# Performance work log

Measured on AMD Instinct MI355X. Metric: run time of the kernel, lower is better.

The kernel has to match this reference:

```python
import jax, jax.numpy as jnp
import numpy as np
import math

N_EMBD = 1024
N_HEAD = 16
HEAD_DIM = N_EMBD // N_HEAD
SEQ = 2048
BATCH = 2
EPS = 1e-5


def _gelu_tanh(x):
    c = math.sqrt(2.0 / math.pi)
    return 0.5 * x * (1.0 + jnp.tanh(c * (x + 0.044715 * x ** 3)))


def _layernorm(x, w, b):
    mean = jnp.mean(x, axis=-1, keepdims=True)
    var = jnp.mean(jnp.square(x - mean), axis=-1, keepdims=True)  # unbiased=False
    return (x - mean) / jnp.sqrt(var + EPS) * w + b


def setup_inputs() -> dict:
    key = jax.random.key(0)
    ks = jax.random.split(key, 8)
    D = N_EMBD
    s = 0.02
    return {
        "x": jax.random.normal(ks[0], (BATCH, SEQ, D), jnp.float32),
        "ln1_w": jnp.ones((D,), jnp.float32),
        "ln1_b": jnp.zeros((D,), jnp.float32),
        "w_qkv": jax.random.normal(ks[1], (D, 3 * D), jnp.float32) * s,
        "b_qkv": jnp.zeros((3 * D,), jnp.float32),
        "w_attn_proj": jax.random.normal(ks[2], (D, D), jnp.float32) * s,
        "b_attn_proj": jnp.zeros((D,), jnp.float32),
        "ln2_w": jnp.ones((D,), jnp.float32),
        "ln2_b": jnp.zeros((D,), jnp.float32),
        "w_fc": jax.random.normal(ks[3], (D, 4 * D), jnp.float32) * s,
        "b_fc": jnp.zeros((4 * D,), jnp.float32),
        "w_proj": jax.random.normal(ks[4], (4 * D, D), jnp.float32) * s,
        "b_proj": jnp.zeros((D,), jnp.float32),
    }


def reference(x, ln1_w, ln1_b, w_qkv, b_qkv, w_attn_proj, b_attn_proj,
              ln2_w, ln2_b, w_fc, b_fc, w_proj, b_proj):
    bs, T, D = x.shape
    # --- attention branch (pre-LN) ---
    h = _layernorm(x, ln1_w, ln1_b)
    qkv = h @ w_qkv + b_qkv                      # [B,T,3D]
    q, k, v = jnp.split(qkv, 3, axis=-1)
    q = q.reshape(bs, T, N_HEAD, HEAD_DIM).transpose(0, 2, 1, 3)  # [B,H,T,d]
    k = k.reshape(bs, T, N_HEAD, HEAD_DIM).transpose(0, 2, 1, 3)
    v = v.reshape(bs, T, N_HEAD, HEAD_DIM).transpose(0, 2, 1, 3)
    scores = jnp.einsum("bhqd,bhkd->bhqk", q, k) * (1.0 / math.sqrt(HEAD_DIM))
    causal = jnp.tril(jnp.ones((T, T), bool))
    scores = jnp.where(causal[None, None], scores, -jnp.inf)
    att = jax.nn.softmax(scores, axis=-1)
    ctx = jnp.einsum("bhqk,bhkd->bhqd", att, v)
    ctx = ctx.transpose(0, 2, 1, 3).reshape(bs, T, D)
    attn_out = ctx @ w_attn_proj + b_attn_proj
    x = x + attn_out
    # --- MLP branch (pre-LN) ---
    h = _layernorm(x, ln2_w, ln2_b)
    h = _gelu_tanh(h @ w_fc + b_fc)
    h = h @ w_proj + b_proj
    return x + h
```

## Files before the change

kernel.cpp:

```cpp
#include <hip/hip_runtime.h>

typedef unsigned short u16;
typedef __attribute__((ext_vector_type(8))) __bf16 bf16x8;
typedef __attribute__((ext_vector_type(8))) unsigned short ushort8;
typedef __attribute__((ext_vector_type(4))) float f32x4;

#define MFMA16(a, b, c) __builtin_amdgcn_mfma_f32_16x16x32_bf16((a), (b), (c), 0, 0, 0)

__device__ __forceinline__ u16 f2bf(float f) {
  union { __bf16 h; u16 u; } cv;
  cv.h = (__bf16)f;
  return cv.u;
}

__device__ __forceinline__ void async16(const u16* g, u16* l) {
  __builtin_amdgcn_global_load_lds(
      (const __attribute__((address_space(1))) void*)g,
      (__attribute__((address_space(3))) void*)l, 16, 0, 0);
}

__global__ __launch_bounds__(256)
void transpose_bf16(const float* __restrict__ W, u16* __restrict__ Wt, int K, int N) {
  __shared__ float t[32][33];
  const int n0 = blockIdx.x * 32, k0 = blockIdx.y * 32;
  const int tx = threadIdx.x, ty = threadIdx.y;
  #pragma unroll
  for (int i = 0; i < 32; i += 8)
    t[ty + i][tx] = W[(size_t)(k0 + ty + i) * N + n0 + tx];
  __syncthreads();
  #pragma unroll
  for (int i = 0; i < 32; i += 8)
    Wt[(size_t)(n0 + ty + i) * K + k0 + tx] = f2bf(t[tx][ty + i]);
}

__global__ __launch_bounds__(256)
void transpose_v(const u16* __restrict__ v, u16* __restrict__ vt) {
  __shared__ u16 t[64][72];
  const int bh = blockIdx.y, t0 = blockIdx.x * 64;
  const int tid = threadIdx.x;
  #pragma unroll
  for (int s = 0; s < 2; ++s) {
    const int idx = tid + s * 256;
    const int row = idx >> 3, ch = idx & 7;
    ushort8 d = *(const ushort8*)(v + ((size_t)bh * 2048 + t0 + row) * 64 + ch * 8);
    #pragma unroll
    for (int e = 0; e < 8; ++e) t[ch * 8 + e][row] = d[e];
  }
  __syncthreads();
  #pragma unroll
  for (int s = 0; s < 2; ++s) {
    const int idx = tid + s * 256;
    const int drow = idx >> 3, ch = idx & 7;
    ushort8 o = *(const ushort8*)(&t[drow][ch * 8]);
    *(ushort8*)(vt + ((size_t)bh * 64 + drow) * 2048 + t0 + ch * 8) = o;
  }
}

__global__ __launch_bounds__(256)
void ln_bf16(const float* __restrict__ X, const float* __restrict__ w,
             const float* __restrict__ bia, u16* __restrict__ out) {
  const int row = blockIdx.x, tid = threadIdx.x;
  const float4 v = ((const float4*)(X + (size_t)row * 1024))[tid];
  float s = v.x + v.y + v.z + v.w;
  float s2 = v.x * v.x + v.y * v.y + v.z * v.z + v.w * v.w;
  #pragma unroll
  for (int o = 32; o > 0; o >>= 1) { s += __shfl_down(s, o); s2 += __shfl_down(s2, o); }
  __shared__ float red[8];
  const int wv = tid >> 6, lane = tid & 63;
  if (lane == 0) { red[wv] = s; red[4 + wv] = s2; }
  __syncthreads();
  s = red[0] + red[1] + red[2] + red[3];
  s2 = red[4] + red[5] + red[6] + red[7];
  const float mean = s * (1.f / 1024.f);
  const float var = s2 * (1.f / 1024.f) - mean * mean;
  const float rstd = rsqrtf(var + 1e-5f);
  const float4 wv4 = ((const float4*)w)[tid];
  const float4 bv4 = ((const float4*)bia)[tid];
  ushort4 o;
  o.x = f2bf((v.x - mean) * rstd * wv4.x + bv4.x);
  o.y = f2bf((v.y - mean) * rstd * wv4.y + bv4.y);
  o.z = f2bf((v.z - mean) * rstd * wv4.z + bv4.z);
  o.w = f2bf((v.w - mean) * rstd * wv4.w + bv4.w);
  ((ushort4*)(out + (size_t)row * 1024))[tid] = o;
}

template <int MODE>
__global__ __launch_bounds__(256)
void gemm_bt(const u16* __restrict__ A, const u16* __restrict__ Bt,
             const float* __restrict__ bias, const float* __restrict__ resid,
             float* __restrict__ outF, u16* __restrict__ outB,
             u16* __restrict__ qo, u16* __restrict__ ko, u16* __restrict__ vo,
             int M, int N, int K, int kSlice) {
  __shared__ u16 As[128 * 64];
  __shared__ u16 Bs[128 * 64];
  const int tid = threadIdx.x;
  const int lane = tid & 63, wv = tid >> 6;
  const int l16 = lane & 15, quad = lane >> 4;
  const int wr = wv >> 1, wc = wv & 1;
  const int m0 = blockIdx.y * 128, n0 = blockIdx.x * 128;
  const int kBegin = blockIdx.z * kSlice, kEnd = kBegin + kSlice;
  const int srow = lane >> 3;
  const int sch = (lane & 7) ^ srow;

  f32x4 acc[4][4];
  const f32x4 fz = {0.f, 0.f, 0.f, 0.f};
  #pragma unroll
  for (int i = 0; i < 4; ++i)
    #pragma unroll
    for (int j = 0; j < 4; ++j) acc[i][j] = fz;

  for (int k0 = kBegin; k0 < kEnd; k0 += 64) {
    __syncthreads();
    #pragma unroll
    for (int s = 0; s < 4; ++s) {
      const int R = wv * 32 + s * 8;
      async16(A + (size_t)(m0 + R + srow) * K + k0 + sch * 8, As + R * 64);
      async16(Bt + (size_t)(n0 + R + srow) * K + k0 + sch * 8, Bs + R * 64);
    }
    __builtin_amdgcn_s_waitcnt(0xF70);
    __syncthreads();
    #pragma unroll
    for (int h = 0; h < 2; ++h) {
      bf16x8 af[4], bfr[4];
      #pragma unroll
      for (int i = 0; i < 4; ++i) {
        const int row = wr * 64 + i * 16 + l16;
        af[i] = *(const bf16x8*)(As + row * 64 + (((h * 4 + quad) ^ (l16 & 7)) * 8));
      }
      #pragma unroll
      for (int j = 0; j < 4; ++j) {
        const int row = wc * 64 + j * 16 + l16;
        bfr[j] = *(const bf16x8*)(Bs + row * 64 + (((h * 4 + quad) ^ (l16 & 7)) * 8));
      }
      #pragma unroll
      for (int i = 0; i < 4; ++i)
        #pragma unroll
        for (int j = 0; j < 4; ++j)
          acc[i][j] = MFMA16(af[i], bfr[j], acc[i][j]);
    }
  }

  #pragma unroll
  for (int i = 0; i < 4; ++i) {
    #pragma unroll
    for (int j = 0; j < 4; ++j) {
      const int col = n0 + wc * 64 + j * 16 + l16;
      const float bc = bias[col];
      #pragma unroll
      for (int r = 0; r < 4; ++r) {
        const int row = m0 + wr * 64 + i * 16 + quad * 4 + r;
        float v = acc[i][j][r];
        if (MODE != 4) v += bc;
        if (MODE == 0) {
          const int which = col >> 10, cc = col & 1023, hh = cc >> 6, dd = cc & 63;
          const int bb = row >> 11, t = row & 2047;
          const u16 bv = f2bf(v);
          const size_t o = ((size_t)(bb * 16 + hh) * 2048 + t) * 64 + dd;
          if (which == 0)
            qo[o] = bv;
          else if (which == 1)
            ko[o] = bv;
          else
            vo[o] = bv;
        } else if (MODE == 1) {
          outF[(size_t)row * N + col] = resid[(size_t)row * N + col] + v;
        } else if (MODE == 2) {
          const float x3 = v * v * v;
          const float u = 0.7978845608028654f * (v + 0.044715f * x3);
          const float e = __expf(2.f * u);
          const float th = 1.f - 2.f / (e + 1.f);
          outB[(size_t)row * N + col] = f2bf(0.5f * v * (1.f + th));
        } else {
          outF[(size_t)blockIdx.z * M * N + (size_t)row * N + col] = v;
        }
      }
    }
  }
}

__global__ __launch_bounds__(256)
void reduce2(const float* __restrict__ P, const float* __restrict__ resid,
             const float* __restrict__ bias, float* __restrict__ out, int MN, int N) {
  const int idx4 = blockIdx.x * 256 + threadIdx.x;
  const size_t s = (size_t)MN >> 2;
  const float4 a = ((const float4*)P)[idx4];
  const float4 b = ((const float4*)P)[idx4 + s];
  const float4 r = ((const float4*)resid)[idx4];
  const float4 bb = ((const float4*)bias)[idx4 & (N / 4 - 1)];
  float4 o;
  o.x = r.x + a.x + b.x + bb.x;
  o.y = r.y + a.y + b.y + bb.y;
  o.z = r.z + a.z + b.z + bb.z;
  o.w = r.w + a.w + b.w + bb.w;
  ((float4*)out)[idx4] = o;
}

__global__ __launch_bounds__(256)
void attn(const u16* __restrict__ Q, const u16* __restrict__ Kg,
          const u16* __restrict__ Vt, u16* __restrict__ ctx) {
  __shared__ u16 Ks[128 * 64];
  __shared__ u16 Vs[64 * 128];
  __shared__ u16 Ps[64 * 128];
  const int px = blockIdx.x;
  const int pair = px >> 1, half = px & 1;
  const int qt0 = pair, qt1 = 15 - pair;
  const int bh = blockIdx.y;
  const int b = bh >> 4, h = bh & 15;
  const int tid = threadIdx.x;
  const int lane = tid & 63, wv = tid >> 6;
  const int l16 = lane & 15, quad = lane >> 4;
  const int rb = half * 64 + wv * 16;
  const float S2 = 0.18033688011112042f;
  const u16* Qb = Q + (size_t)bh * 2048 * 64;
  const u16* Kb = Kg + (size_t)bh * 2048 * 64;
  const u16* Vb = Vt + (size_t)bh * 64 * 2048;

  bf16x8 qf[2][2];
  #pragma unroll
  for (int t = 0; t < 2; ++t)
    #pragma unroll
    for (int c = 0; c < 2; ++c)
      qf[t][c] = *(const bf16x8*)(Qb + (size_t)((t ? qt1 : qt0) * 128 + rb + l16) * 64 +
                                  c * 32 + quad * 8);

  f32x4 octx[2][4];
  const f32x4 fz = {0.f, 0.f, 0.f, 0.f};
  #pragma unroll
  for (int t = 0; t < 2; ++t)
    #pragma unroll
    for (int jd = 0; jd < 4; ++jd) octx[t][jd] = fz;
  float mi2[2] = {-1e30f, -1e30f};
  float li[2] = {0.f, 0.f};

  for (int kt = 0; kt <= qt1; ++kt) {
    __syncthreads();
    #pragma unroll
    for (int s = 0; s < 4; ++s) {
      const int cid = tid + s * 256;
      {
        const int key = cid >> 3, ch = cid & 7;
        ushort8 d = *(const ushort8*)(Kb + (size_t)(kt * 128 + key) * 64 + ch * 8);
        *(ushort8*)(Ks + key * 64 + ((ch ^ (key & 7)) * 8)) = d;
      }
      {
        const int dd = cid >> 4, ch = cid & 15;
        ushort8 d = *(const ushort8*)(Vb + (size_t)dd * 2048 + kt * 128 + ch * 8);
        *(ushort8*)(Vs + dd * 128 + ((ch ^ (dd & 15)) * 8)) = d;
      }
    }
    __syncthreads();

    #pragma unroll
    for (int t = 0; t < 2; ++t) {
      const int qt = t ? qt1 : qt0;
      if (kt > qt) continue;

      f32x4 sa[8];
      #pragma unroll
      for (int j = 0; j < 8; ++j) {
        const int key7 = l16 & 7;
        bf16x8 kf0 = *(const bf16x8*)(Ks + (16 * j + l16) * 64 + ((quad ^ key7) * 8));
        bf16x8 kf1 = *(const bf16x8*)(Ks + (16 * j + l16) * 64 + (((4 + quad) ^ key7) * 8));
        f32x4 tt = MFMA16(kf0, qf[t][0], fz);
        sa[j] = MFMA16(kf1, qf[t][1], tt);
      }
      if (kt == qt) {
        const int rg = rb + l16;
        #pragma unroll
        for (int j = 0; j < 8; ++j)
          #pragma unroll
          for (int r = 0; r < 4; ++r)
            if (j * 16 + quad * 4 + r > rg) sa[j][r] = -1e30f;
      }
      float mx = -1e30f;
      #pragma unroll
      for (int j = 0; j < 8; ++j)
        #pragma unroll
        for (int r = 0; r < 4; ++r) mx = fmaxf(mx, sa[j][r]);
      mx = fmaxf(mx, __shfl_xor(mx, 16));
      mx = fmaxf(mx, __shfl_xor(mx, 32));
      mx *= S2;
      const float mn = fmaxf(mi2[t], mx);
      const float al = __builtin_amdgcn_exp2f(mi2[t] - mn);
      mi2[t] = mn;
      const int row_local = wv * 16 + l16;
      float rs = 0.f;
      #pragma unroll
      for (int j = 0; j < 8; ++j) {
        ushort4 w4;
        float p0 = __builtin_amdgcn_exp2f(sa[j][0] * S2 - mn);
        float p1 = __builtin_amdgcn_exp2f(sa[j][1] * S2 - mn);
        float p2 = __builtin_amdgcn_exp2f(sa[j][2] * S2 - mn);
        float p3 = __builtin_amdgcn_exp2f(sa[j][3] * S2 - mn);
        rs += (p0 + p1) + (p2 + p3);
        w4.x = f2bf(p0); w4.y = f2bf(p1); w4.z = f2bf(p2); w4.w = f2bf(p3);
        const int c = 2 * j + (quad >> 1);
        *(ushort4*)(Ps + row_local * 128 + ((c ^ l16) * 8) + (quad & 1) * 4) = w4;
      }
      rs += __shfl_xor(rs, 16);
      rs += __shfl_xor(rs, 32);
      li[t] = li[t] * al + rs;
      #pragma unroll
      for (int r = 0; r < 4; ++r) {
        const float alr = __shfl(al, quad * 4 + r);
        #pragma unroll
        for (int jd = 0; jd < 4; ++jd) octx[t][jd][r] *= alr;
      }
      #pragma unroll
      for (int c = 0; c < 4; ++c) {
        bf16x8 pf = *(const bf16x8*)(Ps + row_local * 128 + (((c * 4 + quad) ^ l16) * 8));
        #pragma unroll
        for (int jd = 0; jd < 4; ++jd) {
          const int dd = jd * 16 + l16;
          bf16x8 vf = *(const bf16x8*)(Vs + dd * 128 + (((c * 4 + quad) ^ (dd & 15)) * 8));
          octx[t][jd] = MFMA16(pf, vf, octx[t][jd]);
        }
      }
    }
  }
  #pragma unroll
  for (int t = 0; t < 2; ++t) {
    const int qt = t ? qt1 : qt0;
    #pragma unroll
    for (int r = 0; r < 4; ++r) {
      const float lr = __builtin_amdgcn_rcpf(__shfl(li[t], quad * 4 + r));
      const int rowg = qt * 128 + rb + quad * 4 + r;
      #pragma unroll
      for (int jd = 0; jd < 4; ++jd) {
        const int col = h * 64 + jd * 16 + l16;
        ctx[((size_t)b * 2048 + rowg) * 1024 + col] = f2bf(octx[t][jd][r] * lr);
      }
    }
  }
}

extern "C" void kernel_launch(void* const* d_in, const int* in_sizes, int n_in,
                              void* d_out, int out_size, void* d_ws, size_t ws_size,
                              hipStream_t stream) {
  (void)in_sizes; (void)n_in; (void)out_size; (void)ws_size;
  const float* x      = (const float*)d_in[0];
  const float* ln1_w  = (const float*)d_in[1];
  const float* ln1_b  = (const float*)d_in[2];
  const float* w_qkv  = (const float*)d_in[3];
  const float* b_qkv  = (const float*)d_in[4];
  const float* w_attn = (const float*)d_in[5];
  const float* b_attn = (const float*)d_in[6];
  const float* ln2_w  = (const float*)d_in[7];
  const float* ln2_b  = (const float*)d_in[8];
  const float* w_fc   = (const float*)d_in[9];
  const float* b_fc   = (const float*)d_in[10];
  const float* w_proj = (const float*)d_in[11];
  const float* b_proj = (const float*)d_in[12];
  float* out = (float*)d_out;

  char* ws = (char*)d_ws;
  size_t off = 0;
  auto alloc = [&](size_t n) {
    char* p = ws + off;
    off += (n + 255) & ~(size_t)255;
    return p;
  };
  u16* h1     = (u16*)alloc(4096ull * 1024 * 2);
  u16* wqkvT  = (u16*)alloc(3072ull * 1024 * 2);
  u16* wattnT = (u16*)alloc(1024ull * 1024 * 2);
  u16* wfcT   = (u16*)alloc(4096ull * 1024 * 2);
  u16* wprojT = (u16*)alloc(1024ull * 4096 * 2);
  u16* q      = (u16*)alloc(4096ull * 1024 * 2);
  u16* k      = (u16*)alloc(4096ull * 1024 * 2);
  u16* vT     = (u16*)alloc(4096ull * 1024 * 2);
  u16* ctxb   = (u16*)alloc(4096ull * 1024 * 2);
  float* out1 = (float*)alloc(4096ull * 1024 * 4);
  u16* h2     = (u16*)alloc(4096ull * 1024 * 2);
  u16* fco    = (u16*)alloc(4096ull * 4096 * 2);

  u16* vtmp = ctxb;
  float* projP = (float*)q;

  const dim3 tb(32, 8);
  transpose_bf16<<<dim3(3072 / 32, 1024 / 32), tb, 0, stream>>>(w_qkv, wqkvT, 1024, 3072);
  transpose_bf16<<<dim3(1024 / 32, 1024 / 32), tb, 0, stream>>>(w_attn, wattnT, 1024, 1024);
  transpose_bf16<<<dim3(4096 / 32, 1024 / 32), tb, 0, stream>>>(w_fc, wfcT, 1024, 4096);
  transpose_bf16<<<dim3(1024 / 32, 4096 / 32), tb, 0, stream>>>(w_proj, wprojT, 4096, 1024);

  ln_bf16<<<4096, 256, 0, stream>>>(x, ln1_w, ln1_b, h1);

  gemm_bt<0><<<dim3(24, 32, 1), 256, 0, stream>>>(h1, wqkvT, b_qkv, nullptr, nullptr,
                                                  nullptr, q, k, vtmp, 4096, 3072, 1024, 1024);

  transpose_v<<<dim3(32, 32), 256, 0, stream>>>(vtmp, vT);

  attn<<<dim3(16, 32), 256, 0, stream>>>(q, k, vT, ctxb);

  gemm_bt<1><<<dim3(8, 32, 1), 256, 0, stream>>>(ctxb, wattnT, b_attn, x, out1, nullptr,
                                                 nullptr, nullptr, nullptr, 4096, 1024, 1024, 1024);

  ln_bf16<<<4096, 256, 0, stream>>>(out1, ln2_w, ln2_b, h2);

  gemm_bt<2><<<dim3(32, 32, 1), 256, 0, stream>>>(h2, wfcT, b_fc, nullptr, nullptr, fco,
                                                  nullptr, nullptr, nullptr, 4096, 4096, 1024, 1024);

  gemm_bt<4><<<dim3(8, 32, 2), 256, 0, stream>>>(fco, wprojT, b_proj, nullptr, projP, nullptr,
                                                 nullptr, nullptr, nullptr, 4096, 1024, 4096, 2048);

  reduce2<<<4096, 256, 0, stream>>>(projP, out1, b_proj, out, 4096 * 1024, 1024);
}
```

Baseline: 373.7 us.

## Double-buffer K tiles with async LDS loads in attention; split-K attn projection

The attention kernel now stages K into a double-buffered LDS array using global_load_lds async copies, prefetching the next K tile while computing the current one. V is also staged asynchronously, and the softmax and PV work of the two query tiles is interleaved around the barrier to hide load latency. Separately, the attention output projection switches to a split-K GEMM (two partial sums written to scratch) followed by a reduce kernel that adds the residual and bias. This doubles the blocks for that small GEMM, at the cost of an extra kernel and extra fp32 traffic.

```diff
diff --git a/kernel.cpp b/kernel.cpp
--- a/kernel.cpp
+++ b/kernel.cpp
@@ -162,8 +162,6 @@
             ko[o] = bv;
           else
             vo[o] = bv;
-        } else if (MODE == 1) {
-          outF[(size_t)row * N + col] = resid[(size_t)row * N + col] + v;
         } else if (MODE == 2) {
           const float x3 = v * v * v;
           const float u = 0.7978845608028654f * (v + 0.044715f * x3);
@@ -198,7 +196,7 @@
 __global__ __launch_bounds__(256)
 void attn(const u16* __restrict__ Q, const u16* __restrict__ Kg,
           const u16* __restrict__ Vt, u16* __restrict__ ctx) {
-  __shared__ u16 Ks[128 * 64];
+  __shared__ u16 Ks[2][128 * 64];
   __shared__ u16 Vs[64 * 128];
   __shared__ u16 Ps[64 * 128];
   const int px = blockIdx.x;
@@ -210,6 +208,7 @@
   const int lane = tid & 63, wv = tid >> 6;
   const int l16 = lane & 15, quad = lane >> 4;
   const int rb = half * 64 + wv * 16;
+  const int row_local = wv * 16 + l16;
   const float S2 = 0.18033688011112042f;
   const u16* Qb = Q + (size_t)bh * 2048 * 64;
   const u16* Kb = Kg + (size_t)bh * 2048 * 64;
@@ -232,92 +231,120 @@
   float mi2[2] = {-1e30f, -1e30f};
   float li[2] = {0.f, 0.f};
 
-  for (int kt = 0; kt <= qt1; ++kt) {
-    __syncthreads();
+  const int kRow = lane >> 3, kCh = (lane & 7) ^ ((lane >> 3) & 7);
+  const int vRow = lane >> 4;
+  auto stageK = [&](int kt, int buf) {
     #pragma unroll
     for (int s = 0; s < 4; ++s) {
-      const int cid = tid + s * 256;
-      {
-        const int key = cid >> 3, ch = cid & 7;
-        ushort8 d = *(const ushort8*)(Kb + (size_t)(kt * 128 + key) * 64 + ch * 8);
-        *(ushort8*)(Ks + key * 64 + ((ch ^ (key & 7)) * 8)) = d;
-      }
-      {
-        const int dd = cid >> 4, ch = cid & 15;
-        ushort8 d = *(const ushort8*)(Vb + (size_t)dd * 2048 + kt * 128 + ch * 8);
-        *(ushort8*)(Vs + dd * 128 + ((ch ^ (dd & 15)) * 8)) = d;
-      }
-    }
-    __syncthreads();
-
-    #pragma unroll
-    for (int t = 0; t < 2; ++t) {
-      const int qt = t ? qt1 : qt0;
-      if (kt > qt) continue;
-
-      f32x4 sa[8];
-      #pragma unroll
-      for (int j = 0; j < 8; ++j) {
-        const int key7 = l16 & 7;
-        bf16x8 kf0 = *(const bf16x8*)(Ks + (16 * j + l16) * 64 + ((quad ^ key7) * 8));
-        bf16x8 kf1 = *(const bf16x8*)(Ks + (16 * j + l16) * 64 + (((4 + quad) ^ key7) * 8));
-        f32x4 tt = MFMA16(kf0, qf[t][0], fz);
-        sa[j] = MFMA16(kf1, qf[t][1], tt);
-      }
-      if (kt == qt) {
-        const int rg = rb + l16;
-        #pragma unroll
-        for (int j = 0; j < 8; ++j)
-          #pragma unroll
-          for (int r = 0; r < 4; ++r)
-            if (j * 16 + quad * 4 + r > rg) sa[j][r] = -1e30f;
-      }
-      float mx = -1e30f;
+      const int R = wv * 32 + s * 8;
+      async16(Kb + (size_t)(kt * 128 + R + kRow) * 64 + kCh * 8, &Ks[buf][R * 64]);
+    }
+  };
+  auto stageV = [&](int kt) {
+    #pragma unroll
+    for (int s = 0; s < 4; ++s) {
+      const int D = wv * 16 + s * 4;
+      const int dd = D + vRow;
+      const int sch = (lane & 15) ^ (dd & 15);
+      async16(Vb + (size_t)dd * 2048 + kt * 128 + sch * 8, &Vs[D * 128]);
+    }
+  };
+
+  auto softmax_t = [&](int t, f32x4* sa, int kt, int qt) {
+    if (kt == qt) {
+      const int rg = rb + l16;
       #pragma unroll
       for (int j = 0; j < 8; ++j)
         #pragma unroll
-        for (int r = 0; r < 4; ++r) mx = fmaxf(mx, sa[j][r]);
-      mx = fmaxf(mx, __shfl_xor(mx, 16));
-      mx = fmaxf(mx, __shfl_xor(mx, 32));
-      mx *= S2;
-      const float mn = fmaxf(mi2[t], mx);
-      const float al = __builtin_amdgcn_exp2f(mi2[t] - mn);
-      mi2[t] = mn;
-      const int row_local = wv * 16 + l16;
-      float rs = 0.f;
-      #pragma unroll
-      for (int j = 0; j < 8; ++j) {
-        ushort4 w4;
-        float p0 = __builtin_amdgcn_exp2f(sa[j][0] * S2 - mn);
-        float p1 = __builtin_amdgcn_exp2f(sa[j][1] * S2 - mn);
-        float p2 = __builtin_amdgcn_exp2f(sa[j][2] * S2 - mn);
-        float p3 = __builtin_amdgcn_exp2f(sa[j][3] * S2 - mn);
-        rs += (p0 + p1) + (p2 + p3);
-        w4.x = f2bf(p0); w4.y = f2bf(p1); w4.z = f2bf(p2); w4.w = f2bf(p3);
-        const int c = 2 * j + (quad >> 1);
-        *(ushort4*)(Ps + row_local * 128 + ((c ^ l16) * 8) + (quad & 1) * 4) = w4;
+        for (int r = 0; r < 4; ++r)
+          if (j * 16 + quad * 4 + r > rg) sa[j][r] = -1e30f;
+    }
+    float mx = -1e30f;
+    #pragma unroll
+    for (int j = 0; j < 8; ++j)
+      #pragma unroll
+      for (int r = 0; r < 4; ++r) mx = fmaxf(mx, sa[j][r]);
+    mx = fmaxf(mx, __shfl_xor(mx, 16));
+    mx = fmaxf(mx, __shfl_xor(mx, 32));
+    mx *= S2;
+    const float mn = fmaxf(mi2[t], mx);
+    const float al = __builtin_amdgcn_exp2f(mi2[t] - mn);
+    mi2[t] = mn;
+    float rs = 0.f;
+    #pragma unroll
+    for (int j = 0; j < 8; ++j) {
+      ushort4 w4;
+      float p0 = __builtin_amdgcn_exp2f(sa[j][0] * S2 - mn);
+      float p1 = __builtin_amdgcn_exp2f(sa[j][1] * S2 - mn);
+      float p2 = __builtin_amdgcn_exp2f(sa[j][2] * S2 - mn);
+      float p3 = __builtin_amdgcn_exp2f(sa[j][3] * S2 - mn);
+      rs += (p0 + p1) + (p2 + p3);
+      w4.x = f2bf(p0); w4.y = f2bf(p1); w4.z = f2bf(p2); w4.w = f2bf(p3);
+      const int c = 2 * j + (quad >> 1);
+      *(ushort4*)(Ps + row_local * 128 + ((c ^ l16) * 8) + (quad & 1) * 4) = w4;
+    }
+    rs += __shfl_xor(rs, 16);
+    rs += __shfl_xor(rs, 32);
+    li[t] = li[t] * al + rs;
+    #pragma unroll
+    for (int r = 0; r < 4; ++r) {
+      const float alr = __shfl(al, quad * 4 + r);
+      #pragma unroll
+      for (int jd = 0; jd < 4; ++jd) octx[t][jd][r] *= alr;
+    }
+  };
+  auto pv_t = [&](int t) {
+    #pragma unroll
+    for (int c = 0; c < 4; ++c) {
+      bf16x8 pf = *(const bf16x8*)(Ps + row_local * 128 + (((c * 4 + quad) ^ l16) * 8));
+      #pragma unroll
+      for (int jd = 0; jd < 4; ++jd) {
+        const int dd = jd * 16 + l16;
+        bf16x8 vf = *(const bf16x8*)(Vs + dd * 128 + (((c * 4 + quad) ^ (dd & 15)) * 8));
+        octx[t][jd] = MFMA16(pf, vf, octx[t][jd]);
       }
-      rs += __shfl_xor(rs, 16);
-      rs += __shfl_xor(rs, 32);
-      li[t] = li[t] * al + rs;
-      #pragma unroll
-      for (int r = 0; r < 4; ++r) {
-        const float alr = __shfl(al, quad * 4 + r);
-        #pragma unroll
-        for (int jd = 0; jd < 4; ++jd) octx[t][jd][r] *= alr;
-      }
-      #pragma unroll
-      for (int c = 0; c < 4; ++c) {
-        bf16x8 pf = *(const bf16x8*)(Ps + row_local * 128 + (((c * 4 + quad) ^ l16) * 8));
-        #pragma unroll
-        for (int jd = 0; jd < 4; ++jd) {
-          const int dd = jd * 16 + l16;
-          bf16x8 vf = *(const bf16x8*)(Vs + dd * 128 + (((c * 4 + quad) ^ (dd & 15)) * 8));
-          octx[t][jd] = MFMA16(pf, vf, octx[t][jd]);
-        }
-      }
-    }
-  }
+    }
+  };
+
+  stageK(0, 0);
+  __builtin_amdgcn_s_waitcnt(0xF70);
+  __syncthreads();
+
+  for (int kt = 0; kt <= qt1; ++kt) {
+    const int cur = kt & 1;
+    stageV(kt);
+    if (kt < qt1) stageK(kt + 1, cur ^ 1);
+    const bool both = (kt <= qt0);
+
+    f32x4 sa0[8], sa1[8];
+    const u16* KsC = Ks[cur];
+    #pragma unroll
+    for (int j = 0; j < 8; ++j) {
+      const int key7 = l16 & 7;
+      bf16x8 kf0 = *(const bf16x8*)(KsC + (16 * j + l16) * 64 + ((quad ^ key7) * 8));
+      bf16x8 kf1 = *(const bf16x8*)(KsC + (16 * j + l16) * 64 + (((4 + quad) ^ key7) * 8));
+      sa1[j] = MFMA16(kf1, qf[1][1], MFMA16(kf0, qf[1][0], fz));
+      if (both) sa0[j] = MFMA16(kf1, qf[0][1], MFMA16(kf0, qf[0][0], fz));
+    }
+
+    if (both)
+      softmax_t(0, sa0, kt, qt0);
+    else
+      softmax_t(1, sa1, kt, qt1);
+
+    __builtin_amdgcn_s_waitcnt(0xF70);
+    __syncthreads();
+
+    if (both) {
+      pv_t(0);
+      softmax_t(1, sa1, kt, qt1);
+      pv_t(1);
+    } else {
+      pv_t(1);
+    }
+    __syncthreads();
+  }
+
   #pragma unroll
   for (int t = 0; t < 2; ++t) {
     const int qt = t ? qt1 : qt0;
@@ -374,6 +401,7 @@
   u16* fco    = (u16*)alloc(4096ull * 4096 * 2);
 
   u16* vtmp = ctxb;
+  float* apP = (float*)fco;
   float* projP = (float*)q;
 
   const dim3 tb(32, 8);
@@ -391,8 +419,9 @@
 
   attn<<<dim3(16, 32), 256, 0, stream>>>(q, k, vT, ctxb);
 
-  gemm_bt<1><<<dim3(8, 32, 1), 256, 0, stream>>>(ctxb, wattnT, b_attn, x, out1, nullptr,
-                                                 nullptr, nullptr, nullptr, 4096, 1024, 1024, 1024);
+  gemm_bt<4><<<dim3(8, 32, 2), 256, 0, stream>>>(ctxb, wattnT, b_attn, nullptr, apP, nullptr,
+                                                 nullptr, nullptr, nullptr, 4096, 1024, 1024, 512);
+  reduce2<<<4096, 256, 0, stream>>>(apP, x, b_attn, out1, 4096 * 1024, 1024);
 
   ln_bf16<<<4096, 256, 0, stream>>>(out1, ln2_w, ln2_b, h2);
 
```

Result: no change. 372.3 us (-0.4%).
